# Performance work log

Hardware: AMD Instinct MI355X
Metric: run time of the kernel (lower is better)

The kernel has to match this reference:

```python
import jax, jax.numpy as jnp
import numpy as np
from jax import lax

IN_DIM, HID, OUT_DIM = 4, 20, 4
N = 2097152  # batch of collocation points
CHAIN_LENS = (16, 4, 1)


def swish(x):
    return x * jax.nn.sigmoid(x)


def _chain_params(key, length):
    ks = jax.random.split(key, 4)
    s = 0.1
    Wn = jax.random.normal(ks[0], (length, 3, HID, HID), jnp.float32) * s
    bn = jax.random.normal(ks[1], (length, 3, HID), jnp.float32) * s
    Wl = jax.random.normal(ks[2], (length, HID, HID), jnp.float32) * s
    bl = jax.random.normal(ks[3], (length, HID), jnp.float32) * s
    return Wn, bn, Wl, bl


def setup_inputs() -> dict:
    key = jax.random.key(0)
    ks = jax.random.split(key, 8)
    s = 0.1
    inp = {
        "x": jax.random.normal(ks[0], (N, IN_DIM), jnp.float32),
        "front_W": jax.random.normal(ks[1], (IN_DIM, HID), jnp.float32) * s,
        "front_b": jax.random.normal(ks[2], (HID,), jnp.float32) * s,
        "back_W": jax.random.normal(ks[3], (HID, OUT_DIM), jnp.float32) * s,
        "back_b": jax.random.normal(ks[4], (OUT_DIM,), jnp.float32) * s,
    }
    for i, L in enumerate(CHAIN_LENS):
        Wn, bn, Wl, bl = _chain_params(ks[5 + i], L)
        inp[f"Wn{i+1}"], inp[f"bn{i+1}"] = Wn, bn
        inp[f"Wl{i+1}"], inp[f"bl{i+1}"] = Wl, bl
    return inp


def _run_chain(h, Wn, bn, Wl, bl):
    # h: [N, HID]; Wn: [L,3,HID,HID]; bn: [L,3,HID]; Wl: [L,HID,HID]; bl: [L,HID]
    def body(h, p):
        Wn_i, bn_i, Wl_i, bl_i = p
        o = h
        for j in range(3):  # 3 Linear+Swish in block.net
            o = swish(o @ Wn_i[j] + bn_i[j])
        o2 = swish(h @ Wl_i + bl_i)  # block.lin shortcut
        return o + o2, None

    h, _ = lax.scan(body, h, (Wn, bn, Wl, bl))
    return h


def reference(x, front_W, front_b, back_W, back_b,
              Wn1, bn1, Wl1, bl1,
              Wn2, bn2, Wl2, bl2,
              Wn3, bn3, Wl3, bl3):
    h = x @ front_W + front_b  # [N, HID]
    x1 = _run_chain(h, Wn1, bn1, Wl1, bl1)
    x2 = _run_chain(h, Wn2, bn2, Wl2, bl2)
    x3 = _run_chain(h, Wn3, bn3, Wl3, bl3)
    return (x1 + x2 + x3) @ back_W + back_b  # [N, OUT_DIM]
```

## Files before the change

kernel.cpp:

```cpp
#include <hip/hip_runtime.h>
#include <stdint.h>

typedef uint32_t u32;
typedef uint16_t u16;
typedef _Float16 f16;
typedef __attribute__((ext_vector_type(2))) _Float16 h2;
typedef __attribute__((ext_vector_type(8))) _Float16 f16v8;
typedef __attribute__((ext_vector_type(16))) float f32x16;

#define N_MM 86
#define WS_NEED (N_MM * 2048)
#define LOG2E 1.44269504f

#define E0 0x37FE37FEu
#define E1 0xA909A909u
#define E2 0x19011901u
#define ONEF16 0x00003C00u

__device__ __forceinline__ u32 pkf16(float lo, float hi) {
  auto p = __builtin_amdgcn_cvt_pkrtz(lo, hi);
  return __builtin_bit_cast(u32, p);
}
__device__ __forceinline__ h2 uph(u32 v) { return __builtin_bit_cast(h2, v); }
__device__ __forceinline__ u32 phu(h2 v) { return __builtin_bit_cast(u32, v); }
__device__ __forceinline__ u32 pkadd(u32 a, u32 b) { return phu(uph(a) + uph(b)); }

__device__ __forceinline__ f16v8 as_f16(uint4 v) { return __builtin_bit_cast(f16v8, v); }

__device__ __forceinline__ f32x16 zero16() {
  f32x16 z = {0.f, 0.f, 0.f, 0.f, 0.f, 0.f, 0.f, 0.f,
              0.f, 0.f, 0.f, 0.f, 0.f, 0.f, 0.f, 0.f};
  return z;
}

__device__ __forceinline__ void swish5(const f32x16& t, uint4& o, u32& o4) {
  const h2 e0 = uph(E0), e1 = uph(E1), e2 = uph(E2);
  u32 r[5];
#pragma unroll
  for (int i = 0; i < 5; ++i) {
    h2 c = uph(pkf16(t[2 * i], t[2 * i + 1]));
    h2 s = c * c;
    h2 p = __builtin_elementwise_fma(e2, s, e1);
    p = __builtin_elementwise_fma(p, s, e0);
    r[i] = phu(__builtin_elementwise_fma(s, p, c));
  }
  o.x = r[0]; o.y = r[1]; o.z = r[2]; o.w = r[3]; o4 = r[4];
}

__device__ __forceinline__ f32x16 mm2b(uint4 a0, uint4 a1, uint4 b1, uint4 b2, const f32x16& Z) {
  f32x16 acc = __builtin_amdgcn_mfma_f32_32x32x16_f16(as_f16(a0), as_f16(b1), Z, 0, 0, 0);
  acc = __builtin_amdgcn_mfma_f32_32x32x16_f16(as_f16(a1), as_f16(b2), acc, 0, 0, 0);
  return acc;
}

__device__ __forceinline__ u16 f16bits(float v) {
  f16 h = (f16)v;
  return __builtin_bit_cast(u16, h);
}

__global__ void prep_kernel(
    const float* __restrict__ fW, const float* __restrict__ fb,
    const float* __restrict__ bW, const float* __restrict__ bb,
    const float* __restrict__ Wn1, const float* __restrict__ bn1,
    const float* __restrict__ Wl1, const float* __restrict__ bl1,
    const float* __restrict__ Wn2, const float* __restrict__ bn2,
    const float* __restrict__ Wl2, const float* __restrict__ bl2,
    const float* __restrict__ Wn3, const float* __restrict__ bn3,
    const float* __restrict__ Wl3, const float* __restrict__ bl3,
    u32* __restrict__ ws) {
  int mm = blockIdx.x;
  int lane = threadIdx.x;
  int m = lane & 31, g = lane >> 5;
  const float *W, *B;
  int M, Kmax, Mmax;
  float wscale, bscale;
  bool front = (mm == 0);
  if (mm == 0) { W = fW; B = fb; M = 20; Kmax = 4; Mmax = 20; wscale = 2.f; bscale = 2.f; }
  else if (mm == 85) { W = bW; B = bb; M = 4; Kmax = 20; Mmax = 4; wscale = 0.5f; bscale = 1.f; }
  else {
    int idx = mm - 1, bi = idx >> 2, p = idx & 3, lb;
    const int jmap[4] = {0, 3, 1, 2};
    int j = jmap[p];
    const float *Wn, *bn, *Wl, *bl;
    if (bi < 16)      { Wn = Wn1; bn = bn1; Wl = Wl1; bl = bl1; lb = bi; }
    else if (bi < 20) { Wn = Wn2; bn = bn2; Wl = Wl2; bl = bl2; lb = bi - 16; }
    else              { Wn = Wn3; bn = bn3; Wl = Wl3; bl = bl3; lb = 0; }
    if (j < 3) { W = Wn + (lb * 3 + j) * 400; B = bn + (lb * 3 + j) * 20; }
    else       { W = Wl + lb * 400;           B = bl + lb * 20; }
    M = 20; Kmax = 20; Mmax = 20; wscale = 0.5f; bscale = 1.f;
  }
  int ml = (m < 18) ? m : ((m >= 20 && m <= 21) ? m - 2 : -1);
  for (int f = 0; f < 2; ++f) {
    for (int r = 0; r < 4; ++r) {
      u32 v = 0;
      for (int hh = 0; hh < 2; ++hh) {
        int s = 2 * r + hh;
        int k = -1;
        bool bias = false;
        if (front) {
          if (f == 0 && g == 0) {
            if (s < 4) k = s;
            else if (s == 4) bias = true;
          }
        } else {
          if (f == 0) k = 4 * g + s + (s >= 4 ? 4 : 0);
          else if (g == 0) {
            if (s < 2) k = 16 + s;
            else if (s == 4) bias = true;
          } else {
            if (s < 2) k = 18 + s;
          }
        }
        u32 e = 0;
        if (ml >= 0 && ml < Mmax) {
          if (bias) e = f16bits(bscale * B[ml]);
          else if (k >= 0 && k < Kmax) e = f16bits(wscale * W[k * M + ml]);
        }
        v |= e << (16 * hh);
      }
      ws[mm * 512 + f * 256 + lane * 4 + r] = v;
    }
  }
}


#define ROT_PF()  { uint4 nl0 = pf[0], nl1 = pf[64]; pf += 128; \
                    w0 = ca0; w1 = ca1; ca0 = na0; ca1 = na1; na0 = nl0; na1 = nl1; }
#define ROT_NOPF() { w0 = ca0; w1 = ca1; ca0 = na0; ca1 = na1; }

#define BLOCK_BODY(S3ROT)                                                    \
  {                                                                          \
    ROT_PF();                                        \
    f32x16 t0 = mm2b(w0, w1, cb1_0, cb2_0, Z);                               \
    f32x16 t1 = mm2b(w0, w1, cb1_1, cb2_1, Z);                               \
    ROT_PF();         \
    f32x16 u0 = mm2b(w0, w1, cb1_0, cb2_0, Z);                               \
    f32x16 u1 = mm2b(w0, w1, cb1_1, cb2_1, Z);                               \
    swish5(t0, ob1_0, ob2_0.x); swish5(t1, ob1_1, ob2_1.x);                  \
    swish5(u0, pb1_0, p4_0);    swish5(u1, pb1_1, p4_1);                     \
    ROT_PF();                                                     \
    t0 = mm2b(w0, w1, ob1_0, ob2_0, Z);                                      \
    t1 = mm2b(w0, w1, ob1_1, ob2_1, Z);                                      \
    swish5(t0, ob1_0, ob2_0.x); swish5(t1, ob1_1, ob2_1.x);                  \
    S3ROT();                                                      \
    t0 = mm2b(w0, w1, ob1_0, ob2_0, Z);                                      \
    t1 = mm2b(w0, w1, ob1_1, ob2_1, Z);                                      \
    swish5(t0, ob1_0, ob2_0.x); swish5(t1, ob1_1, ob2_1.x);                  \
    cb1_0.x = pkadd(ob1_0.x, pb1_0.x);                                       \
    cb1_0.y = pkadd(ob1_0.y, pb1_0.y);                                       \
    cb1_0.z = pkadd(ob1_0.z, pb1_0.z);                                       \
    cb1_0.w = pkadd(ob1_0.w, pb1_0.w);                                       \
    cb2_0.x = pkadd(ob2_0.x, p4_0);                                          \
    cb1_1.x = pkadd(ob1_1.x, pb1_1.x);                                       \
    cb1_1.y = pkadd(ob1_1.y, pb1_1.y);                                       \
    cb1_1.z = pkadd(ob1_1.z, pb1_1.z);                                       \
    cb1_1.w = pkadd(ob1_1.w, pb1_1.w);                                       \
    cb2_1.x = pkadd(ob2_1.x, p4_1);                                          \
  }

__global__ __launch_bounds__(256) void reslinear_mfma(
    const float* __restrict__ x, const uint4* __restrict__ ws4,
    float* __restrict__ out, int ntiles2) {
  int lane = threadIdx.x & 63;
  int wave = threadIdx.x >> 6;
  int tile2 = blockIdx.x * 4 + wave;
  if (tile2 >= ntiles2) return;
  int n = lane & 31;
  bool hi = lane >= 32;
  int pt0 = tile2 * 64 + n;
  int pt1 = pt0 + 32;

  const f32x16 Z = zero16();
  const uint4* __restrict__ wlane = ws4 + lane;

  uint4 af  = wlane[0];
  uint4 ca0 = wlane[128], ca1 = wlane[192];
  uint4 na0 = wlane[256], na1 = wlane[320];
  const uint4* __restrict__ pf = wlane + 384;
  uint4 w0, w1;

  float4 x0 = ((const float4*)x)[pt0];
  float4 x1 = ((const float4*)x)[pt1];
  uint4 bfr0, bfr1;
  bfr0.x = pkf16(x0.x, x0.y); bfr0.y = pkf16(x0.z, x0.w); bfr0.z = ONEF16; bfr0.w = 0u;
  bfr1.x = pkf16(x1.x, x1.y); bfr1.y = pkf16(x1.z, x1.w); bfr1.z = ONEF16; bfr1.w = 0u;
  f32x16 t0 = __builtin_amdgcn_mfma_f32_32x32x16_f16(as_f16(af), as_f16(bfr0), Z, 0, 0, 0);
  f32x16 t1 = __builtin_amdgcn_mfma_f32_32x32x16_f16(as_f16(af), as_f16(bfr1), Z, 0, 0, 0);
  u32 h0[5], h1[5];
#pragma unroll
  for (int i = 0; i < 5; ++i) h0[i] = pkf16(t0[2 * i], t0[2 * i + 1]);
#pragma unroll
  for (int i = 0; i < 5; ++i) h1[i] = pkf16(t1[2 * i], t1[2 * i + 1]);

  u32 as0[5], as1[5];
#pragma unroll
  for (int i = 0; i < 5; ++i) { as0[i] = 0u; as1[i] = 0u; }

  uint4 cb1_0, cb2_0, ob1_0, ob2_0, pb1_0;
  uint4 cb1_1, cb2_1, ob1_1, ob2_1, pb1_1;
  u32 p4_0, p4_1;
  cb2_0.y = 0u; cb2_0.z = ONEF16; cb2_0.w = 0u;
  cb2_1.y = 0u; cb2_1.z = ONEF16; cb2_1.w = 0u;
  ob2_0.y = 0u; ob2_0.z = ONEF16; ob2_0.w = 0u;
  ob2_1.y = 0u; ob2_1.z = ONEF16; ob2_1.w = 0u;

  const int CH_L2[2] = {16, 4};

  for (int c = 0; c < 2; ++c) {
    cb1_0.x = h0[0]; cb1_0.y = h0[1]; cb1_0.z = h0[2]; cb1_0.w = h0[3]; cb2_0.x = h0[4];
    cb1_1.x = h1[0]; cb1_1.y = h1[1]; cb1_1.z = h1[2]; cb1_1.w = h1[3]; cb2_1.x = h1[4];
    int L = CH_L2[c];
    for (int b = 0; b < L; ++b) {
      BLOCK_BODY(ROT_PF)
    }
    as0[0] = pkadd(as0[0], cb1_0.x);
    as0[1] = pkadd(as0[1], cb1_0.y);
    as0[2] = pkadd(as0[2], cb1_0.z);
    as0[3] = pkadd(as0[3], cb1_0.w);
    as0[4] = pkadd(as0[4], cb2_0.x);
    as1[0] = pkadd(as1[0], cb1_1.x);
    as1[1] = pkadd(as1[1], cb1_1.y);
    as1[2] = pkadd(as1[2], cb1_1.z);
    as1[3] = pkadd(as1[3], cb1_1.w);
    as1[4] = pkadd(as1[4], cb2_1.x);
  }

  {
    cb1_0.x = h0[0]; cb1_0.y = h0[1]; cb1_0.z = h0[2]; cb1_0.w = h0[3]; cb2_0.x = h0[4];
    cb1_1.x = h1[0]; cb1_1.y = h1[1]; cb1_1.z = h1[2]; cb1_1.w = h1[3]; cb2_1.x = h1[4];
    BLOCK_BODY(ROT_NOPF)
    as0[0] = pkadd(as0[0], cb1_0.x);
    as0[1] = pkadd(as0[1], cb1_0.y);
    as0[2] = pkadd(as0[2], cb1_0.z);
    as0[3] = pkadd(as0[3], cb1_0.w);
    as0[4] = pkadd(as0[4], cb2_0.x);
    as1[0] = pkadd(as1[0], cb1_1.x);
    as1[1] = pkadd(as1[1], cb1_1.y);
    as1[2] = pkadd(as1[2], cb1_1.z);
    as1[3] = pkadd(as1[3], cb1_1.w);
    as1[4] = pkadd(as1[4], cb2_1.x);
  }

  {
    cb1_0.x = as0[0]; cb1_0.y = as0[1]; cb1_0.z = as0[2]; cb1_0.w = as0[3]; cb2_0.x = as0[4];
    cb1_1.x = as1[0]; cb1_1.y = as1[1]; cb1_1.z = as1[2]; cb1_1.w = as1[3]; cb2_1.x = as1[4];
    f32x16 r0 = mm2b(ca0, ca1, cb1_0, cb2_0, Z);
    f32x16 r1 = mm2b(ca0, ca1, cb1_1, cb2_1, Z);
    if (!hi) {
      ((float4*)out)[pt0] = make_float4(r0[0], r0[1], r0[2], r0[3]);
      ((float4*)out)[pt1] = make_float4(r1[0], r1[1], r1[2], r1[3]);
    }
  }
}

__device__ __forceinline__ float fast_exp2(float x) {
#if __has_builtin(__builtin_amdgcn_exp2f)
  return __builtin_amdgcn_exp2f(x);
#else
  return exp2f(x);
#endif
}
__device__ __forceinline__ float fast_rcp(float x) {
#if __has_builtin(__builtin_amdgcn_rcpf)
  return __builtin_amdgcn_rcpf(x);
#else
  return 1.0f / x;
#endif
}
__device__ __forceinline__ float swish_f(float x) {
  float e = fast_exp2(x * -LOG2E);
  return x * fast_rcp(1.0f + e);
}
__device__ __forceinline__ void matvec20f(float* __restrict__ t, const float* __restrict__ o,
                                          const float* __restrict__ W, const float* __restrict__ b) {
#pragma unroll
  for (int l = 0; l < 20; ++l) t[l] = b[l];
#pragma unroll
  for (int k = 0; k < 20; ++k) {
    float ok = o[k];
#pragma unroll
    for (int l = 0; l < 20; ++l) t[l] = fmaf(ok, W[k * 20 + l], t[l]);
  }
}
__global__ __launch_bounds__(256) void reslinear_fallback(
    const float* __restrict__ x, const float* __restrict__ fW, const float* __restrict__ fb,
    const float* __restrict__ bW, const float* __restrict__ bb,
    const float* __restrict__ Wn1, const float* __restrict__ bn1, const float* __restrict__ Wl1, const float* __restrict__ bl1,
    const float* __restrict__ Wn2, const float* __restrict__ bn2, const float* __restrict__ Wl2, const float* __restrict__ bl2,
    const float* __restrict__ Wn3, const float* __restrict__ bn3, const float* __restrict__ Wl3, const float* __restrict__ bl3,
    float* __restrict__ out, int np) {
  int tid = blockIdx.x * 256 + threadIdx.x;
  if (tid >= np) return;
  float4 d = ((const float4*)x)[tid];
  float xv[4] = {d.x, d.y, d.z, d.w};
  float h[20];
#pragma unroll
  for (int l = 0; l < 20; ++l) h[l] = fb[l];
#pragma unroll
  for (int k = 0; k < 4; ++k)
#pragma unroll
    for (int l = 0; l < 20; ++l) h[l] = fmaf(xv[k], fW[k * 20 + l], h[l]);
  float acc[20];
#pragma unroll
  for (int l = 0; l < 20; ++l) acc[l] = 0.f;
  for (int c = 0; c < 3; ++c) {
    const float* Wn = (c == 0) ? Wn1 : ((c == 1) ? Wn2 : Wn3);
    const float* bn = (c == 0) ? bn1 : ((c == 1) ? bn2 : bn3);
    const float* Wl = (c == 0) ? Wl1 : ((c == 1) ? Wl2 : Wl3);
    const float* bl = (c == 0) ? bl1 : ((c == 1) ? bl2 : bl3);
    const int L = (c == 0) ? 16 : ((c == 1) ? 4 : 1);
    float hc[20];
#pragma unroll
    for (int l = 0; l < 20; ++l) hc[l] = h[l];
    for (int i = 0; i < L; ++i) {
      float o[20], t[20];
#pragma unroll
      for (int l = 0; l < 20; ++l) o[l] = hc[l];
      for (int j = 0; j < 3; ++j) {
        matvec20f(t, o, Wn + j * 400, bn + j * 20);
#pragma unroll
        for (int l = 0; l < 20; ++l) o[l] = swish_f(t[l]);
      }
      matvec20f(t, hc, Wl, bl);
#pragma unroll
      for (int l = 0; l < 20; ++l) hc[l] = o[l] + swish_f(t[l]);
      Wn += 1200; bn += 60; Wl += 400; bl += 20;
    }
#pragma unroll
    for (int l = 0; l < 20; ++l) acc[l] += hc[l];
  }
  float r[4];
#pragma unroll
  for (int j = 0; j < 4; ++j) r[j] = bb[j];
#pragma unroll
  for (int k = 0; k < 20; ++k)
#pragma unroll
    for (int j = 0; j < 4; ++j) r[j] = fmaf(acc[k], bW[k * 4 + j], r[j]);
  ((float4*)out)[tid] = make_float4(r[0], r[1], r[2], r[3]);
}

extern "C" void kernel_launch(void* const* d_in, const int* in_sizes, int n_in,
                              void* d_out, int out_size, void* d_ws, size_t ws_size,
                              hipStream_t stream) {
  int np = in_sizes[0] / 4;

  if (ws_size >= (size_t)WS_NEED && (np % 64) == 0) {
    prep_kernel<<<N_MM, 64, 0, stream>>>(
        (const float*)d_in[1], (const float*)d_in[2], (const float*)d_in[3], (const float*)d_in[4],
        (const float*)d_in[5], (const float*)d_in[6], (const float*)d_in[7], (const float*)d_in[8],
        (const float*)d_in[9], (const float*)d_in[10], (const float*)d_in[11], (const float*)d_in[12],
        (const float*)d_in[13], (const float*)d_in[14], (const float*)d_in[15], (const float*)d_in[16],
        (u32*)d_ws);
    int ntiles2 = np / 64;
    int blocks = (ntiles2 + 3) / 4;
    reslinear_mfma<<<blocks, 256, 0, stream>>>(
        (const float*)d_in[0], (const uint4*)d_ws, (float*)d_out, ntiles2);
  } else {
    reslinear_fallback<<<(np + 255) / 256, 256, 0, stream>>>(
        (const float*)d_in[0], (const float*)d_in[1], (const float*)d_in[2], (const float*)d_in[3],
        (const float*)d_in[4], (const float*)d_in[5], (const float*)d_in[6], (const float*)d_in[7],
        (const float*)d_in[8], (const float*)d_in[9], (const float*)d_in[10], (const float*)d_in[11],
        (const float*)d_in[12], (const float*)d_in[13], (const float*)d_in[14], (const float*)d_in[15],
        (const float*)d_in[16], (float*)d_out, np);
  }
}
```

Before: 533.6 us.

## Stage per-block weights through double-buffered LDS shared by all waves

Replaces the per-wave register rotation that prefetched each block's MFMA weight fragments from global memory with a block-cooperative, double-buffered LDS stage. All 256 threads load the next residual block's 4 weight matrices into shared memory while the current block computes, then synchronize. Each wave reads its fragments from LDS, so the four waves no longer each fetch the same weights from global/L2. The cost is a __syncthreads per residual block and extra LDS traffic, and inactive waves can no longer exit early.

```diff
diff --git a/kernel.cpp b/kernel.cpp
--- a/kernel.cpp
+++ b/kernel.cpp
@@ -124,25 +124,22 @@
 }
 
 
-#define ROT_PF()  { uint4 nl0 = pf[0], nl1 = pf[64]; pf += 128; \
-                    w0 = ca0; w1 = ca1; ca0 = na0; ca1 = na1; na0 = nl0; na1 = nl1; }
-#define ROT_NOPF() { w0 = ca0; w1 = ca1; ca0 = na0; ca1 = na1; }
-
-#define BLOCK_BODY(S3ROT)                                                    \
+#define BLOCK_BODY()                                                         \
   {                                                                          \
-    ROT_PF();                                        \
+    const uint4* __restrict__ wb = &wsh[buf][0][0][lane];                    \
+    uint4 w0 = wb[0], w1 = wb[64];                                \
     f32x16 t0 = mm2b(w0, w1, cb1_0, cb2_0, Z);                               \
     f32x16 t1 = mm2b(w0, w1, cb1_1, cb2_1, Z);                               \
-    ROT_PF();         \
+    w0 = wb[128]; w1 = wb[192];              \
     f32x16 u0 = mm2b(w0, w1, cb1_0, cb2_0, Z);                               \
     f32x16 u1 = mm2b(w0, w1, cb1_1, cb2_1, Z);                               \
     swish5(t0, ob1_0, ob2_0.x); swish5(t1, ob1_1, ob2_1.x);                  \
     swish5(u0, pb1_0, p4_0);    swish5(u1, pb1_1, p4_1);                     \
-    ROT_PF();                                                     \
+    w0 = wb[256]; w1 = wb[320];                                   \
     t0 = mm2b(w0, w1, ob1_0, ob2_0, Z);                                      \
     t1 = mm2b(w0, w1, ob1_1, ob2_1, Z);                                      \
     swish5(t0, ob1_0, ob2_0.x); swish5(t1, ob1_1, ob2_1.x);                  \
-    S3ROT();                                                      \
+    w0 = wb[384]; w1 = wb[448];                                   \
     t0 = mm2b(w0, w1, ob1_0, ob2_0, Z);                                      \
     t1 = mm2b(w0, w1, ob1_1, ob2_1, Z);                                      \
     swish5(t0, ob1_0, ob2_0.x); swish5(t1, ob1_1, ob2_1.x);                  \
@@ -161,26 +158,31 @@
 __global__ __launch_bounds__(256) void reslinear_mfma(
     const float* __restrict__ x, const uint4* __restrict__ ws4,
     float* __restrict__ out, int ntiles2) {
-  int lane = threadIdx.x & 63;
-  int wave = threadIdx.x >> 6;
+  __shared__ uint4 wsh[2][4][2][64];
+  int tid = threadIdx.x;
+  int lane = tid & 63;
+  int wave = tid >> 6;
   int tile2 = blockIdx.x * 4 + wave;
-  if (tile2 >= ntiles2) return;
+  bool active = tile2 < ntiles2;
+  int t2 = active ? tile2 : 0;
   int n = lane & 31;
   bool hi = lane >= 32;
-  int pt0 = tile2 * 64 + n;
+  int pt0 = t2 * 64 + n;
   int pt1 = pt0 + 32;
 
   const f32x16 Z = zero16();
   const uint4* __restrict__ wlane = ws4 + lane;
 
-  uint4 af  = wlane[0];
-  uint4 ca0 = wlane[128], ca1 = wlane[192];
-  uint4 na0 = wlane[256], na1 = wlane[320];
-  const uint4* __restrict__ pf = wlane + 384;
-  uint4 w0, w1;
+  {
+    uint4 s0 = ws4[128 + tid];
+    uint4 s1 = ws4[384 + tid];
+    ((uint4*)wsh)[tid] = s0;
+    ((uint4*)wsh)[tid + 256] = s1;
+  }
 
   float4 x0 = ((const float4*)x)[pt0];
   float4 x1 = ((const float4*)x)[pt1];
+  uint4 af = wlane[0];
   uint4 bfr0, bfr1;
   bfr0.x = pkf16(x0.x, x0.y); bfr0.y = pkf16(x0.z, x0.w); bfr0.z = ONEF16; bfr0.w = 0u;
   bfr1.x = pkf16(x1.x, x1.y); bfr1.y = pkf16(x1.z, x1.w); bfr1.z = ONEF16; bfr1.w = 0u;
@@ -191,6 +193,8 @@
   for (int i = 0; i < 5; ++i) h0[i] = pkf16(t0[2 * i], t0[2 * i + 1]);
 #pragma unroll
   for (int i = 0; i < 5; ++i) h1[i] = pkf16(t1[2 * i], t1[2 * i + 1]);
+
+  __syncthreads();
 
   u32 as0[5], as1[5];
 #pragma unroll
@@ -204,14 +208,31 @@
   ob2_0.y = 0u; ob2_0.z = ONEF16; ob2_0.w = 0u;
   ob2_1.y = 0u; ob2_1.z = ONEF16; ob2_1.w = 0u;
 
-  const int CH_L2[2] = {16, 4};
-
-  for (int c = 0; c < 2; ++c) {
+  const int CH_L[3] = {16, 4, 1};
+
+  int g = 0, buf = 0;
+  for (int c = 0; c < 3; ++c) {
     cb1_0.x = h0[0]; cb1_0.y = h0[1]; cb1_0.z = h0[2]; cb1_0.w = h0[3]; cb2_0.x = h0[4];
     cb1_1.x = h1[0]; cb1_1.y = h1[1]; cb1_1.z = h1[2]; cb1_1.w = h1[3]; cb2_1.x = h1[4];
-    int L = CH_L2[c];
+    int L = CH_L[c];
     for (int b = 0; b < L; ++b) {
-      BLOCK_BODY(ROT_PF)
+      bool do_stage = (g + 1) < 21;
+      uint4 s0, s1;
+      if (do_stage) {
+        const uint4* __restrict__ src = ws4 + (size_t)(1 + (g + 1) * 4) * 128 + tid;
+        s0 = src[0];
+        s1 = src[256];
+      }
+
+      BLOCK_BODY()
+
+      if (do_stage) {
+        ((uint4*)wsh)[(buf ^ 1) * 512 + tid] = s0;
+        ((uint4*)wsh)[(buf ^ 1) * 512 + tid + 256] = s1;
+      }
+      __syncthreads();
+      buf ^= 1;
+      ++g;
     }
     as0[0] = pkadd(as0[0], cb1_0.x);
     as0[1] = pkadd(as0[1], cb1_0.y);
@@ -226,27 +247,13 @@
   }
 
   {
-    cb1_0.x = h0[0]; cb1_0.y = h0[1]; cb1_0.z = h0[2]; cb1_0.w = h0[3]; cb2_0.x = h0[4];
-    cb1_1.x = h1[0]; cb1_1.y = h1[1]; cb1_1.z = h1[2]; cb1_1.w = h1[3]; cb2_1.x = h1[4];
-    BLOCK_BODY(ROT_NOPF)
-    as0[0] = pkadd(as0[0], cb1_0.x);
-    as0[1] = pkadd(as0[1], cb1_0.y);
-    as0[2] = pkadd(as0[2], cb1_0.z);
-    as0[3] = pkadd(as0[3], cb1_0.w);
-    as0[4] = pkadd(as0[4], cb2_0.x);
-    as1[0] = pkadd(as1[0], cb1_1.x);
-    as1[1] = pkadd(as1[1], cb1_1.y);
-    as1[2] = pkadd(as1[2], cb1_1.z);
-    as1[3] = pkadd(as1[3], cb1_1.w);
-    as1[4] = pkadd(as1[4], cb2_1.x);
-  }
-
-  {
+    uint4 a0 = wlane[85 * 128];
+    uint4 a1 = wlane[85 * 128 + 64];
     cb1_0.x = as0[0]; cb1_0.y = as0[1]; cb1_0.z = as0[2]; cb1_0.w = as0[3]; cb2_0.x = as0[4];
     cb1_1.x = as1[0]; cb1_1.y = as1[1]; cb1_1.z = as1[2]; cb1_1.w = as1[3]; cb2_1.x = as1[4];
-    f32x16 r0 = mm2b(ca0, ca1, cb1_0, cb2_0, Z);
-    f32x16 r1 = mm2b(ca0, ca1, cb1_1, cb2_1, Z);
-    if (!hi) {
+    f32x16 r0 = mm2b(a0, a1, cb1_0, cb2_0, Z);
+    f32x16 r1 = mm2b(a0, a1, cb1_1, cb2_1, Z);
+    if (active && !hi) {
       ((float4*)out)[pt0] = make_float4(r0[0], r0[1], r0[2], r0[3]);
       ((float4*)out)[pt1] = make_float4(r1[0], r1[1], r1[2], r1[3]);
     }
```

Result: slower. 555.3 us (+4.1%).
